# Performance work log

Measured on AMD Instinct MI355X. Metric: run time of the kernel, lower is better.

The kernel has to match this reference:

```python
import jax, jax.numpy as jnp
import numpy as np
import math

NUM_HEADS = 16


def setup_inputs() -> dict:
    key = jax.random.key(0)
    ks = jax.random.split(key, 7)
    d_model = 2048
    b, s = 2, 2048
    h = NUM_HEADS
    dh = d_model // h
    past_len = 2048
    std = math.sqrt(2.0 / (d_model + d_model))
    def w(k):
        return std * jax.random.truncated_normal(k, -3.0, 3.0, (d_model, d_model), jnp.float32)
    return {
        "x": jax.random.normal(ks[0], (b, s, d_model), jnp.float32),
        "past_k": jax.random.normal(ks[1], (b * h, past_len, dh), jnp.float32),
        "past_v": jax.random.normal(ks[2], (b * h, past_len, dh), jnp.float32),
        "Wq": w(ks[3]),
        "Wk": w(ks[4]),
        "Wv": w(ks[5]),
        "Wo": w(ks[6]),
    }


def reference(x, past_k, past_v, Wq, Wk, Wv, Wo):
    b, s, d_model = x.shape
    h = NUM_HEADS
    dh = d_model // h

    def proj_split(W):
        # (b, s, d_model) -> (b*h, s, dh)
        y = jnp.einsum('bsd,od->bso', x, W)
        return y.reshape(b, s, h, dh).transpose(0, 2, 1, 3).reshape(b * h, s, dh)

    Q = proj_split(Wq)
    K = proj_split(Wk)
    V = proj_split(Wv)

    past_len = past_k.shape[1]
    K = jnp.concatenate([past_k, K], axis=1)  # (b*h, total, dh)
    V = jnp.concatenate([past_v, V], axis=1)
    total = past_len + s

    # causal mask: query i (absolute pos past_len+i) attends to keys j <= past_len+i
    qi = jnp.arange(s)[:, None]
    kj = jnp.arange(total)[None, :]
    mask = kj <= (qi + past_len)  # (s, total)

    scores = jnp.einsum('bqd,bkd->bqk', Q, K) / math.sqrt(dh)
    scores = jnp.where(mask[None], scores, -jnp.inf)
    weights = jax.nn.softmax(scores, axis=-1)
    attn = jnp.einsum('bqk,bkv->bqv', weights, V)  # (b*h, s, dh)

    attn = attn.reshape(b, h, s, dh).transpose(0, 2, 1, 3).reshape(b, s, d_model)
    out = jnp.einsum('bsd,od->bso', attn, Wo)
    return out, K, V
```

## Files before the change

### kernel.cpp

```cpp
#include <hip/hip_runtime.h>

#define DM    2048
#define PAST  2048
#define TOT   4096
#define SCALE 0.08838834764831845f

typedef __attribute__((ext_vector_type(8))) short bf16x8;
typedef __attribute__((ext_vector_type(4))) float f32x4;
typedef __attribute__((ext_vector_type(4))) short s16x4;

typedef __attribute__((address_space(1))) void gvoid;
typedef __attribute__((address_space(3))) void lvoid;

__device__ __forceinline__ void gload16(const void* g, void* l) {
  __builtin_amdgcn_global_load_lds((gvoid*)g, (lvoid*)l, 16, 0, 0);
}

__device__ __forceinline__ short f2b(float f) {
  unsigned u = __float_as_uint(f);
  u += 0x7fffu + ((u >> 16) & 1u);
  return (short)(u >> 16);
}

__device__ __forceinline__ unsigned pk2(float a, float b) {
  return (unsigned)(unsigned short)f2b(a) | ((unsigned)(unsigned short)f2b(b) << 16);
}

template <bool F>
__device__ __forceinline__ bf16x8 ld8(const void* base, size_t eidx) {
  if constexpr (F) {
    const float* p = (const float*)base + eidx;
    float4 a = *(const float4*)p;
    float4 b = *(const float4*)(p + 4);
    bf16x8 r;
    r[0] = f2b(a.x); r[1] = f2b(a.y); r[2] = f2b(a.z); r[3] = f2b(a.w);
    r[4] = f2b(b.x); r[5] = f2b(b.y); r[6] = f2b(b.z); r[7] = f2b(b.w);
    return r;
  } else {
    return *(const bf16x8*)((const short*)base + eidx);
  }
}

__global__ void detect_dtype(const unsigned short* __restrict__ w, int* flag) {
  int cnt = 0;
#pragma unroll
  for (int i = 0; i < 4; ++i) {
    unsigned short v = w[i * 64 + threadIdx.x];
    int e = (v >> 7) & 0xFF;
    cnt += (e >= 126) ? 1 : 0;
  }
  for (int off = 32; off; off >>= 1) cnt += __shfl_down(cnt, off);
  if (threadIdx.x == 0) *flag = (cnt >= 8) ? 1 : 0;
}

__global__ __launch_bounds__(256)
void to_bf16(const int* __restrict__ flag,
             const float* __restrict__ x,
             const float* __restrict__ wq, const float* __restrict__ wk,
             const float* __restrict__ wv, const float* __restrict__ wo,
             short* __restrict__ xb, short* __restrict__ wqb,
             short* __restrict__ wkb, short* __restrict__ wvb,
             short* __restrict__ wob) {
  if (*flag != 1) return;
  const float* src; short* dst; size_t off = 0;
  switch (blockIdx.z) {
    case 0: src = x;  dst = xb;  break;
    case 1: src = x;  dst = xb;  off = 4194304; break;
    case 2: src = wq; dst = wqb; break;
    case 3: src = wk; dst = wkb; break;
    case 4: src = wv; dst = wvb; break;
    default: src = wo; dst = wob; break;
  }
  const size_t i = off + ((size_t)blockIdx.x * 256 + threadIdx.x) * 8;
  *(bf16x8*)(dst + i) = ld8<true>(src, i);
}

__device__ __forceinline__ void gemm_mainloop(
    const short* __restrict__ Ab, const short* __restrict__ Wb,
    short* shA, short* shB, f32x4 acc[4][4]) {
  const int tid  = threadIdx.x;
  const int lane = tid & 63, wid = tid >> 6;
  const int ln = lane & 15, qd = lane >> 4;
  const int wr = wid >> 1, wc = wid & 1;

  const int srow = lane >> 3;
  const int scol = ((lane & 7) ^ (lane >> 3)) * 8;

  for (int k0 = 0; k0 < DM; k0 += 64) {
#pragma unroll
    for (int i = 0; i < 4; ++i) {
      const int r8 = (wid * 4 + i) * 8 + srow;
      gload16(Ab + (size_t)r8 * DM + k0 + scol, (char*)shA + (wid * 4 + i) * 1024);
      gload16(Wb + (size_t)r8 * DM + k0 + scol, (char*)shB + (wid * 4 + i) * 1024);
    }
    __syncthreads();

#pragma unroll
    for (int t = 0; t < 2; ++t) {
      bf16x8 af[4], bw[4];
#pragma unroll
      for (int i = 0; i < 4; ++i) {
        const int rowA = wr * 64 + i * 16 + ln;
        const int rowB = wc * 64 + i * 16 + ln;
        const int cb   = ((t << 2) + qd) << 4;
        af[i] = *(const bf16x8*)((const char*)shA + rowA * 128 + (cb ^ ((rowA & 7) << 4)));
        bw[i] = *(const bf16x8*)((const char*)shB + rowB * 128 + (cb ^ ((rowB & 7) << 4)));
      }
#pragma unroll
      for (int i = 0; i < 4; ++i)
#pragma unroll
        for (int j = 0; j < 4; ++j)
          acc[i][j] = __builtin_amdgcn_mfma_f32_16x16x32_bf16(af[i], bw[j], acc[i][j], 0, 0, 0);
    }
    __syncthreads();
  }
}

__global__ __launch_bounds__(256, 2)
void qkv_gemm(const int* __restrict__ flag,
              const short* __restrict__ x0, const short* __restrict__ x1,
              const short* __restrict__ wq0, const short* __restrict__ wk0,
              const short* __restrict__ wv0,
              const short* __restrict__ wq1, const short* __restrict__ wk1,
              const short* __restrict__ wv1,
              short* __restrict__ Qws,
              short* __restrict__ Kb, float* __restrict__ Kf,
              short* __restrict__ Vb, float* __restrict__ Vf) {
  __shared__ __align__(16) short shA[128 * 64];
  __shared__ __align__(16) short shB[128 * 64];
  const int isF = *flag;
  const int bm = blockIdx.y, bn = blockIdx.x;
  const int seg = bn >> 4, bnl = bn & 15;

  const short* A = isF ? x1 : x0;
  const short* W = (seg == 0) ? (isF ? wq1 : wq0)
                  : (seg == 1) ? (isF ? wk1 : wk0)
                               : (isF ? wv1 : wv0);

  const f32x4 fz = {0.f, 0.f, 0.f, 0.f};
  f32x4 acc[4][4];
#pragma unroll
  for (int i = 0; i < 4; ++i)
#pragma unroll
    for (int j = 0; j < 4; ++j) acc[i][j] = fz;

  gemm_mainloop(A + (size_t)bm * 128 * DM, W + (size_t)bnl * 128 * DM, shA, shB, acc);

  const int tid  = threadIdx.x;
  const int lane = tid & 63, wid = tid >> 6;
  const int ln = lane & 15, qd = lane >> 4;
  const int wr = wid >> 1, wc = wid & 1;

#pragma unroll
  for (int i = 0; i < 4; ++i) {
    const int rbase = bm * 128 + wr * 64 + i * 16 + qd * 4;
#pragma unroll
    for (int j = 0; j < 4; ++j) {
      const int col = bnl * 128 + wc * 64 + j * 16 + ln;
#pragma unroll
      for (int r = 0; r < 4; ++r) {
        const int rr = rbase + r;
        const int bb = rr >> 11, sq = rr & 2047;
        const int hh = col >> 7, dd = col & 127;
        float v = acc[i][j][r];
        if (seg == 0) {
          const size_t idx = (((size_t)bb * 16 + hh) * 2048 + sq) * 128 + dd;
          Qws[idx] = f2b(v * SCALE);
        } else {
          const size_t idx = (((size_t)bb * 16 + hh) * (size_t)TOT + PAST + sq) * 128 + dd;
          if (seg == 1) { if (isF) Kf[idx] = v; else Kb[idx] = f2b(v); }
          else          { if (isF) Vf[idx] = v; else Vb[idx] = f2b(v); }
        }
      }
    }
  }
}

__global__ __launch_bounds__(256, 2)
void out_gemm(const int* __restrict__ flag,
              const short* __restrict__ A,
              const short* __restrict__ wo0, const short* __restrict__ wo1,
              void* __restrict__ dst) {
  __shared__ __align__(16) short shA[128 * 64];
  __shared__ __align__(16) short shB[128 * 64];
  const int isF = *flag;
  const int bm = blockIdx.y, bn = blockIdx.x;
  const short* W = isF ? wo1 : wo0;

  const f32x4 fz = {0.f, 0.f, 0.f, 0.f};
  f32x4 acc[4][4];
#pragma unroll
  for (int i = 0; i < 4; ++i)
#pragma unroll
    for (int j = 0; j < 4; ++j) acc[i][j] = fz;

  gemm_mainloop(A + (size_t)bm * 128 * DM, W + (size_t)bn * 128 * DM, shA, shB, acc);

  const int tid  = threadIdx.x;
  const int lane = tid & 63, wid = tid >> 6;
  const int ln = lane & 15, qd = lane >> 4;
  const int wr = wid >> 1, wc = wid & 1;

#pragma unroll
  for (int i = 0; i < 4; ++i) {
    const int rbase = bm * 128 + wr * 64 + i * 16 + qd * 4;
#pragma unroll
    for (int j = 0; j < 4; ++j) {
      const int col = bn * 128 + wc * 64 + j * 16 + ln;
#pragma unroll
      for (int r = 0; r < 4; ++r) {
        const size_t idx = (size_t)(rbase + r) * DM + col;
        if (isF) ((float*)dst)[idx] = acc[i][j][r];
        else     ((short*)dst)[idx] = f2b(acc[i][j][r]);
      }
    }
  }
}

__global__ __launch_bounds__(256)
void copy_past(const int* __restrict__ flag,
               const void* __restrict__ pk, const void* __restrict__ pv,
               short* __restrict__ Kb, float* __restrict__ Kf,
               short* __restrict__ Vb, float* __restrict__ Vf) {
  const int isF = *flag;
  const void* src = blockIdx.z ? pv : pk;
  const size_t c = (size_t)blockIdx.x * 256 + threadIdx.x;
  const size_t bh = c >> 15;
  const size_t rem = c & 32767;
  const size_t si = c * 8, di = bh * (size_t)TOT * 128 + rem * 8;
  if (isF) {
    float* dst = blockIdx.z ? Vf : Kf;
    const float* s = (const float*)src + si;
    float4 a = *(const float4*)s, b = *(const float4*)(s + 4);
    *(float4*)(dst + di) = a; *(float4*)(dst + di + 4) = b;
  } else {
    short* dst = blockIdx.z ? Vb : Kb;
    *(bf16x8*)(dst + di) = *(const bf16x8*)((const short*)src + si);
  }
}

__global__ __launch_bounds__(256)
void transpose_v(const int* __restrict__ flag,
                 const short* __restrict__ Vb, const float* __restrict__ Vf,
                 short* __restrict__ Vt) {
  __shared__ __align__(16) short sh[64 * 136];
  const int isF = *flag;
  const int tid = threadIdx.x;
  const int bh = blockIdx.y, kb = blockIdx.x << 6;
  const int krow = tid >> 4, dc = tid & 15;
#pragma unroll
  for (int rnd = 0; rnd < 4; ++rnd) {
    const int key = rnd * 16 + krow;
    const size_t idx = ((size_t)bh * TOT + kb + key) * 128 + dc * 8;
    bf16x8 v = isF ? ld8<true>(Vf, idx) : ld8<false>(Vb, idx);
    *(bf16x8*)(sh + key * 136 + dc * 8) = v;
  }
  __syncthreads();
  short* dstb = Vt + (size_t)bh * 128 * TOT + kb;
  const int drow = tid >> 3, keyc = tid & 7;
#pragma unroll
  for (int rnd = 0; rnd < 4; ++rnd) {
    const int dr = rnd * 32 + drow;
    bf16x8 ov;
#pragma unroll
    for (int e = 0; e < 8; ++e) ov[e] = sh[(keyc * 8 + e) * 136 + dr];
    *(bf16x8*)(dstb + (size_t)dr * TOT + keyc * 8) = ov;
  }
}

template <bool F>
__global__ __launch_bounds__(256, 2)
void attn_kernel(const int* __restrict__ flag, int want,
                 const short* __restrict__ Q,
                 const void* __restrict__ K,
                 const short* __restrict__ Vt,
                 short* __restrict__ attn) {
  if (*flag != want) return;
  __shared__ __align__(16) short shK[64 * 136];
  __shared__ __align__(16) short shV[128 * 72];
  __shared__ __align__(16) short shP[4][32 * 72];

  const int tid = threadIdx.x;
  const int lane = tid & 63, wid = tid >> 6;
  const int ln = lane & 15, qd = lane >> 4;

  const int l = blockIdx.y * 16 + blockIdx.x;
  const int qt = l >> 5;
  const int bh = ((l & 7) << 2) | ((l >> 3) & 3);
  const int q0 = qt << 7;
  const int r0w = q0 + wid * 32;

  bf16x8 qf[2][4];
#pragma unroll
  for (int mi = 0; mi < 2; ++mi) {
    const short* Qb = Q + ((size_t)bh * 2048 + r0w + mi * 16 + ln) * 128;
#pragma unroll
    for (int t = 0; t < 4; ++t) qf[mi][t] = *(const bf16x8*)(Qb + t * 32 + qd * 8);
  }

  const f32x4 fz = {0.f, 0.f, 0.f, 0.f};
  f32x4 O[2][8];
#pragma unroll
  for (int mi = 0; mi < 2; ++mi)
#pragma unroll
    for (int dt = 0; dt < 8; ++dt) O[mi][dt] = fz;
  float m_i[2] = {-1e30f, -1e30f}, l_i[2] = {0.f, 0.f};

  const short* Vb = Vt + (size_t)bh * 128 * TOT;
  const int ntiles = 34 + 2 * qt;

  const int krow = tid >> 4, kcol = tid & 15;
  const int vrow = tid >> 3, vcol = tid & 7;
  short* shPw = &shP[wid][0];

  bf16x8 vk[4], vv[4];
#pragma unroll
  for (int rnd = 0; rnd < 4; ++rnd) {
    vk[rnd] = ld8<F>(K, ((size_t)bh * TOT + rnd * 16 + krow) * 128 + kcol * 8);
    vv[rnd] = *(const bf16x8*)(Vb + (size_t)(rnd * 32 + vrow) * TOT + vcol * 8);
  }

  for (int kt = 0; kt < ntiles; ++kt) {
    const int kb = kt << 6;
#pragma unroll
    for (int rnd = 0; rnd < 4; ++rnd) {
      *(bf16x8*)(shK + (rnd * 16 + krow) * 136 + kcol * 8) = vk[rnd];
      *(bf16x8*)(shV + (rnd * 32 + vrow) * 72 + vcol * 8) = vv[rnd];
    }
    __syncthreads();

    if (kt + 1 < ntiles) {
      const int nb = kb + 64;
#pragma unroll
      for (int rnd = 0; rnd < 4; ++rnd) {
        vk[rnd] = ld8<F>(K, ((size_t)bh * TOT + nb + rnd * 16 + krow) * 128 + kcol * 8);
        vv[rnd] = *(const bf16x8*)(Vb + (size_t)(rnd * 32 + vrow) * TOT + nb + vcol * 8);
      }
    }

    f32x4 sacc[2][4];
#pragma unroll
    for (int mi = 0; mi < 2; ++mi)
#pragma unroll
      for (int j = 0; j < 4; ++j) sacc[mi][j] = fz;
#pragma unroll
    for (int t = 0; t < 4; ++t) {
#pragma unroll
      for (int j = 0; j < 4; ++j) {
        bf16x8 kf = *(const bf16x8*)(shK + (j * 16 + ln) * 136 + ((t << 2) + qd) * 8);
        sacc[0][j] = __builtin_amdgcn_mfma_f32_16x16x32_bf16(kf, qf[0][t], sacc[0][j], 0, 0, 0);
        sacc[1][j] = __builtin_amdgcn_mfma_f32_16x16x32_bf16(kf, qf[1][t], sacc[1][j], 0, 0, 0);
      }
    }

    const bool maskt = (kt >= ntiles - 2);

#pragma unroll
    for (int mi = 0; mi < 2; ++mi) {
      const int q = r0w + mi * 16 + ln;
      float vmax = -1e30f;
      if (maskt) {
        const int lim = PAST + q;
#pragma unroll
        for (int j = 0; j < 4; ++j)
#pragma unroll
          for (int r = 0; r < 4; ++r) {
            const int kj = kb + j * 16 + qd * 4 + r;
            float s = sacc[mi][j][r];
            s = (kj <= lim) ? s : -1e30f;
            sacc[mi][j][r] = s;
            vmax = fmaxf(vmax, s);
          }
      } else {
#pragma unroll
        for (int j = 0; j < 4; ++j)
#pragma unroll
          for (int r = 0; r < 4; ++r) vmax = fmaxf(vmax, sacc[mi][j][r]);
      }
      vmax = fmaxf(vmax, __shfl_xor(vmax, 16));
      vmax = fmaxf(vmax, __shfl_xor(vmax, 32));
      const float mold = m_i[mi];
      const bool renew = vmax > mold;
      const float mnew = renew ? vmax : mold;
      float rsum = 0.f;
#pragma unroll
      for (int j = 0; j < 4; ++j)
#pragma unroll
        for (int r = 0; r < 4; ++r) {
          const float p = __expf(sacc[mi][j][r] - mnew);
          sacc[mi][j][r] = p;
          rsum += p;
        }
      rsum += __shfl_xor(rsum, 16);
      rsum += __shfl_xor(rsum, 32);
      if (renew) {
        const float alpha = __expf(mold - mnew);
        m_i[mi] = mnew;
        l_i[mi] = l_i[mi] * alpha + rsum;
#pragma unroll
        for (int dt = 0; dt < 8; ++dt) O[mi][dt] *= alpha;
      } else {
        l_i[mi] += rsum;
      }
      const int qr = mi * 16 + ln;
#pragma unroll
      for (int j = 0; j < 4; ++j) {
        uint2 w;
        w.x = pk2(sacc[mi][j][0], sacc[mi][j][1]);
        w.y = pk2(sacc[mi][j][2], sacc[mi][j][3]);
        *(uint2*)(shPw + qr * 72 + j * 16 + qd * 4) = w;
      }
    }

#pragma unroll
    for (int tk = 0; tk < 2; ++tk) {
      bf16x8 pf[2];
#pragma unroll
      for (int mi = 0; mi < 2; ++mi)
        pf[mi] = *(const bf16x8*)(shPw + (mi * 16 + ln) * 72 + ((tk << 2) + qd) * 8);
#pragma unroll
      for (int dt = 0; dt < 8; ++dt) {
        bf16x8 vf = *(const bf16x8*)(shV + (dt * 16 + ln) * 72 + ((tk << 2) + qd) * 8);
        O[0][dt] = __builtin_amdgcn_mfma_f32_16x16x32_bf16(vf, pf[0], O[0][dt], 0, 0, 0);
        O[1][dt] = __builtin_amdgcn_mfma_f32_16x16x32_bf16(vf, pf[1], O[1][dt], 0, 0, 0);
      }
    }
    __syncthreads();
  }

  const int bb = bh >> 4, hh = bh & 15;
#pragma unroll
  for (int mi = 0; mi < 2; ++mi) {
    const float inv = 1.0f / l_i[mi];
    const int q = r0w + mi * 16 + ln;
    short* dst = attn + ((size_t)bb * 2048 + q) * DM + hh * 128;
#pragma unroll
    for (int dt = 0; dt < 8; ++dt) {
      s16x4 o;
#pragma unroll
      for (int r = 0; r < 4; ++r) o[r] = f2b(O[mi][dt][r] * inv);
      *(s16x4*)(dst + dt * 16 + qd * 4) = o;
    }
  }
}

extern "C" void kernel_launch(void* const* d_in, const int* in_sizes, int n_in,
                              void* d_out, int out_size, void* d_ws, size_t ws_size,
                              hipStream_t stream) {
  (void)in_sizes; (void)n_in; (void)out_size; (void)ws_size;
  const void* x  = d_in[0];
  const void* pk = d_in[1];
  const void* pv = d_in[2];
  const void* Wq = d_in[3];
  const void* Wk = d_in[4];
  const void* Wv = d_in[5];
  const void* Wo = d_in[6];

  int* flag = (int*)d_ws;
  short* base = (short*)((char*)d_ws + 256);
  short* Qws    = base;
  short* attnws = base + 8388608;
  short* xb     = attnws;
  short* Vtws   = base + 16777216;
  short* wqb    = Vtws;
  short* wkb    = Vtws + 4194304;
  short* wvb    = Vtws + 8388608;
  short* wob    = base + 33554432;

  short* outB  = (short*)d_out;
  short* KoutB = outB + (size_t)8388608;
  short* VoutB = KoutB + (size_t)16777216;
  float* outF  = (float*)d_out;
  float* KoutF = outF + (size_t)8388608;
  float* VoutF = KoutF + (size_t)16777216;

  dim3 blk(256);
  detect_dtype<<<1, 64, 0, stream>>>((const unsigned short*)Wq, flag);

  to_bf16<<<dim3(2048, 1, 6), blk, 0, stream>>>(flag,
      (const float*)x, (const float*)Wq, (const float*)Wk, (const float*)Wv,
      (const float*)Wo, xb, wqb, wkb, wvb, wob);

  qkv_gemm<<<dim3(48, 32), blk, 0, stream>>>(flag,
      (const short*)x, xb,
      (const short*)Wq, (const short*)Wk, (const short*)Wv,
      wqb, wkb, wvb,
      Qws, KoutB, KoutF, VoutB, VoutF);

  copy_past<<<dim3(4096, 1, 2), blk, 0, stream>>>(flag, pk, pv,
      KoutB, KoutF, VoutB, VoutF);

  transpose_v<<<dim3(64, 32), blk, 0, stream>>>(flag, VoutB, VoutF, Vtws);

  attn_kernel<false><<<dim3(16, 32), blk, 0, stream>>>(flag, 0, Qws, KoutB, Vtws, attnws);
  attn_kernel<true ><<<dim3(16, 32), blk, 0, stream>>>(flag, 1, Qws, KoutF, Vtws, attnws);

  out_gemm<<<dim3(16, 32), blk, 0, stream>>>(flag, attnws, (const short*)Wo, wob, d_out);
}
```

Baseline: 639.7 us.

## Double-buffer GEMM mainloop with larger tiles, hardware bf16 pack, reorder attention blocks

Replaces the GEMM mainloop with a double-buffered pipeline over 32-wide K steps, using 512-thread blocks and larger 256x256 (QKV) and 128x256 (output) tiles, so global loads overlap MFMA work. Software bf16 rounding is replaced by the v_cvt_pk_bf16_f32 instruction throughout. The attention grid mapping is changed to balance causal work across the launch order. The online softmax now only rescales when the running max grows by more than 8, which skips rescaling work but relies on exp values staying bounded. The new LDS layout has no swizzle, so bank conflicts on fragment reads are possible.

```diff
diff --git a/kernel.cpp b/kernel.cpp
--- a/kernel.cpp
+++ b/kernel.cpp
@@ -22,8 +22,10 @@
   return (short)(u >> 16);
 }
 
-__device__ __forceinline__ unsigned pk2(float a, float b) {
-  return (unsigned)(unsigned short)f2b(a) | ((unsigned)(unsigned short)f2b(b) << 16);
+__device__ __forceinline__ unsigned cvtpk(float lo, float hi) {
+  unsigned r;
+  asm("v_cvt_pk_bf16_f32 %0, %1, %2" : "=v"(r) : "v"(lo), "v"(hi));
+  return r;
 }
 
 template <bool F>
@@ -32,10 +34,10 @@
     const float* p = (const float*)base + eidx;
     float4 a = *(const float4*)p;
     float4 b = *(const float4*)(p + 4);
-    bf16x8 r;
-    r[0] = f2b(a.x); r[1] = f2b(a.y); r[2] = f2b(a.z); r[3] = f2b(a.w);
-    r[4] = f2b(b.x); r[5] = f2b(b.y); r[6] = f2b(b.z); r[7] = f2b(b.w);
-    return r;
+    union { unsigned u[4]; bf16x8 v; } r;
+    r.u[0] = cvtpk(a.x, a.y); r.u[1] = cvtpk(a.z, a.w);
+    r.u[2] = cvtpk(b.x, b.y); r.u[3] = cvtpk(b.z, b.w);
+    return r.v;
   } else {
     return *(const bf16x8*)((const short*)base + eidx);
   }
@@ -75,48 +77,66 @@
   *(bf16x8*)(dst + i) = ld8<true>(src, i);
 }
 
-__device__ __forceinline__ void gemm_mainloop(
-    const short* __restrict__ Ab, const short* __restrict__ Wb,
-    short* shA, short* shB, f32x4 acc[4][4]) {
-  const int tid  = threadIdx.x;
+template <int BM>
+__device__ __forceinline__ void pipe_main(const short* __restrict__ A,
+                                          const short* __restrict__ W,
+                                          short* sA, short* sB,
+                                          f32x4 acc[][4]) {
+  constexpr int MF = BM / 32;
+  constexpr int NL = BM / 128 + 2;
+  const int tid = threadIdx.x;
   const int lane = tid & 63, wid = tid >> 6;
   const int ln = lane & 15, qd = lane >> 4;
-  const int wr = wid >> 1, wc = wid & 1;
-
-  const int srow = lane >> 3;
-  const int scol = ((lane & 7) ^ (lane >> 3)) * 8;
-
-  for (int k0 = 0; k0 < DM; k0 += 64) {
-#pragma unroll
-    for (int i = 0; i < 4; ++i) {
-      const int r8 = (wid * 4 + i) * 8 + srow;
-      gload16(Ab + (size_t)r8 * DM + k0 + scol, (char*)shA + (wid * 4 + i) * 1024);
-      gload16(Wb + (size_t)r8 * DM + k0 + scol, (char*)shB + (wid * 4 + i) * 1024);
-    }
-    __syncthreads();
-
-#pragma unroll
-    for (int t = 0; t < 2; ++t) {
-      bf16x8 af[4], bw[4];
-#pragma unroll
-      for (int i = 0; i < 4; ++i) {
-        const int rowA = wr * 64 + i * 16 + ln;
-        const int rowB = wc * 64 + i * 16 + ln;
-        const int cb   = ((t << 2) + qd) << 4;
-        af[i] = *(const bf16x8*)((const char*)shA + rowA * 128 + (cb ^ ((rowA & 7) << 4)));
-        bw[i] = *(const bf16x8*)((const char*)shB + rowB * 128 + (cb ^ ((rowB & 7) << 4)));
-      }
-#pragma unroll
-      for (int i = 0; i < 4; ++i)
-#pragma unroll
-        for (int j = 0; j < 4; ++j)
-          acc[i][j] = __builtin_amdgcn_mfma_f32_16x16x32_bf16(af[i], bw[j], acc[i][j], 0, 0, 0);
-    }
-    __syncthreads();
-  }
-}
-
-__global__ __launch_bounds__(256, 2)
+  const int wm = wid >> 2, wn = wid & 3;
+
+  const int srow = tid >> 2;
+  const int scol = (tid & 3) * 8;
+
+  auto stage = [&](int t, int buf) {
+    const int k0 = t * 32;
+#pragma unroll
+    for (int c = 0; c < BM / 128; ++c)
+      gload16(A + (size_t)(c * 128 + srow) * DM + k0 + scol,
+              (char*)sA + buf * (BM * 64) + c * 8192 + tid * 16);
+#pragma unroll
+    for (int c = 0; c < 2; ++c)
+      gload16(W + (size_t)(c * 128 + srow) * DM + k0 + scol,
+              (char*)sB + buf * 16384 + c * 8192 + tid * 16);
+  };
+
+  stage(0, 0);
+  stage(1, 1);
+  asm volatile("s_waitcnt vmcnt(%0)" :: "n"(NL) : "memory");
+  __builtin_amdgcn_s_barrier();
+
+  for (int t = 0; t < 64; ++t) {
+    const short* Ab = sA + (t & 1) * (BM * 32);
+    const short* Bb = sB + (t & 1) * 8192;
+    bf16x8 af[MF], bw[4];
+#pragma unroll
+    for (int j = 0; j < 4; ++j)
+      bw[j] = *(const bf16x8*)(Bb + (wn * 64 + j * 16 + ln) * 32 + qd * 8);
+#pragma unroll
+    for (int i = 0; i < MF; ++i)
+      af[i] = *(const bf16x8*)(Ab + (wm * (BM / 2) + i * 16 + ln) * 32 + qd * 8);
+#pragma unroll
+    for (int i = 0; i < MF; ++i)
+#pragma unroll
+      for (int j = 0; j < 4; ++j)
+        acc[i][j] = __builtin_amdgcn_mfma_f32_16x16x32_bf16(af[i], bw[j], acc[i][j], 0, 0, 0);
+    if (t == 63) break;
+    __builtin_amdgcn_s_barrier();
+    if (t + 2 < 64) {
+      stage(t + 2, t & 1);
+      asm volatile("s_waitcnt vmcnt(%0)" :: "n"(NL) : "memory");
+    } else {
+      asm volatile("s_waitcnt vmcnt(0)" ::: "memory");
+    }
+    __builtin_amdgcn_s_barrier();
+  }
+}
+
+__global__ __launch_bounds__(512, 2)
 void qkv_gemm(const int* __restrict__ flag,
               const short* __restrict__ x0, const short* __restrict__ x1,
               const short* __restrict__ wq0, const short* __restrict__ wk0,
@@ -126,37 +146,37 @@
               short* __restrict__ Qws,
               short* __restrict__ Kb, float* __restrict__ Kf,
               short* __restrict__ Vb, float* __restrict__ Vf) {
-  __shared__ __align__(16) short shA[128 * 64];
-  __shared__ __align__(16) short shB[128 * 64];
+  __shared__ __align__(16) short sA[2 * 256 * 32];
+  __shared__ __align__(16) short sB[2 * 256 * 32];
   const int isF = *flag;
   const int bm = blockIdx.y, bn = blockIdx.x;
-  const int seg = bn >> 4, bnl = bn & 15;
-
-  const short* A = isF ? x1 : x0;
-  const short* W = (seg == 0) ? (isF ? wq1 : wq0)
-                  : (seg == 1) ? (isF ? wk1 : wk0)
-                               : (isF ? wv1 : wv0);
+  const int seg = bn >> 3, bnl = bn & 7;
+
+  const short* A = (isF ? x1 : x0) + (size_t)bm * 256 * DM;
+  const short* W = ((seg == 0) ? (isF ? wq1 : wq0)
+                   : (seg == 1) ? (isF ? wk1 : wk0)
+                                : (isF ? wv1 : wv0)) + (size_t)bnl * 256 * DM;
 
   const f32x4 fz = {0.f, 0.f, 0.f, 0.f};
-  f32x4 acc[4][4];
-#pragma unroll
-  for (int i = 0; i < 4; ++i)
+  f32x4 acc[8][4];
+#pragma unroll
+  for (int i = 0; i < 8; ++i)
 #pragma unroll
     for (int j = 0; j < 4; ++j) acc[i][j] = fz;
 
-  gemm_mainloop(A + (size_t)bm * 128 * DM, W + (size_t)bnl * 128 * DM, shA, shB, acc);
-
-  const int tid  = threadIdx.x;
+  pipe_main<256>(A, W, sA, sB, acc);
+
+  const int tid = threadIdx.x;
   const int lane = tid & 63, wid = tid >> 6;
   const int ln = lane & 15, qd = lane >> 4;
-  const int wr = wid >> 1, wc = wid & 1;
-
-#pragma unroll
-  for (int i = 0; i < 4; ++i) {
-    const int rbase = bm * 128 + wr * 64 + i * 16 + qd * 4;
+  const int wm = wid >> 2, wn = wid & 3;
+
+#pragma unroll
+  for (int i = 0; i < 8; ++i) {
+    const int rbase = bm * 256 + wm * 128 + i * 16 + qd * 4;
 #pragma unroll
     for (int j = 0; j < 4; ++j) {
-      const int col = bnl * 128 + wc * 64 + j * 16 + ln;
+      const int col = bnl * 256 + wn * 64 + j * 16 + ln;
 #pragma unroll
       for (int r = 0; r < 4; ++r) {
         const int rr = rbase + r;
@@ -176,16 +196,16 @@
   }
 }
 
-__global__ __launch_bounds__(256, 2)
+__global__ __launch_bounds__(512, 2)
 void out_gemm(const int* __restrict__ flag,
               const short* __restrict__ A,
               const short* __restrict__ wo0, const short* __restrict__ wo1,
               void* __restrict__ dst) {
-  __shared__ __align__(16) short shA[128 * 64];
-  __shared__ __align__(16) short shB[128 * 64];
+  __shared__ __align__(16) short sA[2 * 128 * 32];
+  __shared__ __align__(16) short sB[2 * 256 * 32];
   const int isF = *flag;
   const int bm = blockIdx.y, bn = blockIdx.x;
-  const short* W = isF ? wo1 : wo0;
+  const short* W = (isF ? wo1 : wo0) + (size_t)bn * 256 * DM;
 
   const f32x4 fz = {0.f, 0.f, 0.f, 0.f};
   f32x4 acc[4][4];
@@ -194,19 +214,19 @@
 #pragma unroll
     for (int j = 0; j < 4; ++j) acc[i][j] = fz;
 
-  gemm_mainloop(A + (size_t)bm * 128 * DM, W + (size_t)bn * 128 * DM, shA, shB, acc);
-
-  const int tid  = threadIdx.x;
+  pipe_main<128>(A + (size_t)bm * 128 * DM, W, sA, sB, acc);
+
+  const int tid = threadIdx.x;
   const int lane = tid & 63, wid = tid >> 6;
   const int ln = lane & 15, qd = lane >> 4;
-  const int wr = wid >> 1, wc = wid & 1;
+  const int wm = wid >> 2, wn = wid & 3;
 
 #pragma unroll
   for (int i = 0; i < 4; ++i) {
-    const int rbase = bm * 128 + wr * 64 + i * 16 + qd * 4;
+    const int rbase = bm * 128 + wm * 64 + i * 16 + qd * 4;
 #pragma unroll
     for (int j = 0; j < 4; ++j) {
-      const int col = bn * 128 + wc * 64 + j * 16 + ln;
+      const int col = bn * 256 + wn * 64 + j * 16 + ln;
 #pragma unroll
       for (int r = 0; r < 4; ++r) {
         const size_t idx = (size_t)(rbase + r) * DM + col;
@@ -285,8 +305,9 @@
   const int ln = lane & 15, qd = lane >> 4;
 
   const int l = blockIdx.y * 16 + blockIdx.x;
-  const int qt = l >> 5;
-  const int bh = ((l & 7) << 2) | ((l >> 3) & 3);
+  const int s = l >> 3;
+  const int qt = (s < 32) ? (s >> 2) : (15 - ((s - 32) >> 2));
+  const int bh = ((l & 7) << 2) | (s & 3);
   const int q0 = qt << 7;
   const int r0w = q0 + wid * 32;
 
@@ -366,10 +387,10 @@
 #pragma unroll
           for (int r = 0; r < 4; ++r) {
             const int kj = kb + j * 16 + qd * 4 + r;
-            float s = sacc[mi][j][r];
-            s = (kj <= lim) ? s : -1e30f;
-            sacc[mi][j][r] = s;
-            vmax = fmaxf(vmax, s);
+            float v = sacc[mi][j][r];
+            v = (kj <= lim) ? v : -1e30f;
+            sacc[mi][j][r] = v;
+            vmax = fmaxf(vmax, v);
           }
       } else {
 #pragma unroll
@@ -380,7 +401,7 @@
       vmax = fmaxf(vmax, __shfl_xor(vmax, 16));
       vmax = fmaxf(vmax, __shfl_xor(vmax, 32));
       const float mold = m_i[mi];
-      const bool renew = vmax > mold;
+      const bool renew = vmax > mold + 8.0f;
       const float mnew = renew ? vmax : mold;
       float rsum = 0.f;
 #pragma unroll
@@ -406,8 +427,8 @@
 #pragma unroll
       for (int j = 0; j < 4; ++j) {
         uint2 w;
-        w.x = pk2(sacc[mi][j][0], sacc[mi][j][1]);
-        w.y = pk2(sacc[mi][j][2], sacc[mi][j][3]);
+        w.x = cvtpk(sacc[mi][j][0], sacc[mi][j][1]);
+        w.y = cvtpk(sacc[mi][j][2], sacc[mi][j][3]);
         *(uint2*)(shPw + qr * 72 + j * 16 + qd * 4) = w;
       }
     }
@@ -436,10 +457,10 @@
     short* dst = attn + ((size_t)bb * 2048 + q) * DM + hh * 128;
 #pragma unroll
     for (int dt = 0; dt < 8; ++dt) {
-      s16x4 o;
-#pragma unroll
-      for (int r = 0; r < 4; ++r) o[r] = f2b(O[mi][dt][r] * inv);
-      *(s16x4*)(dst + dt * 16 + qd * 4) = o;
+      union { unsigned u[2]; s16x4 v; } o;
+      o.u[0] = cvtpk(O[mi][dt][0] * inv, O[mi][dt][1] * inv);
+      o.u[1] = cvtpk(O[mi][dt][2] * inv, O[mi][dt][3] * inv);
+      *(s16x4*)(dst + dt * 16 + qd * 4) = o.v;
     }
   }
 }
@@ -481,7 +502,7 @@
       (const float*)x, (const float*)Wq, (const float*)Wk, (const float*)Wv,
       (const float*)Wo, xb, wqb, wkb, wvb, wob);
 
-  qkv_gemm<<<dim3(48, 32), blk, 0, stream>>>(flag,
+  qkv_gemm<<<dim3(24, 16), dim3(512), 0, stream>>>(flag,
       (const short*)x, xb,
       (const short*)Wq, (const short*)Wk, (const short*)Wv,
       wqb, wkb, wvb,
@@ -495,5 +516,6 @@
   attn_kernel<false><<<dim3(16, 32), blk, 0, stream>>>(flag, 0, Qws, KoutB, Vtws, attnws);
   attn_kernel<true ><<<dim3(16, 32), blk, 0, stream>>>(flag, 1, Qws, KoutF, Vtws, attnws);
 
-  out_gemm<<<dim3(16, 32), blk, 0, stream>>>(flag, attnws, (const short*)Wo, wob, d_out);
-}
+  out_gemm<<<dim3(8, 32), dim3(512), 0, stream>>>(flag, attnws,
+      (const short*)Wo, wob, d_out);
+}
```

After: 741.6 us. +15.9%, slower.

## Double-buffer GEMM LDS, use hardware exp2 and packed bf16 converts, rebalance attention tiles

Applied to the files above, without the earlier changes.

The GEMM main loop now uses two LDS buffers, prefetching the next K-slice while the current one is multiplied, so each iteration waits on one barrier instead of two. The attention softmax folds log2(e) into the Q scale and calls hardware v_exp_f32 directly. It also rescales the running max only when the new max exceeds the old by more than 8 (lazy rescale). Software bf16 rounding is replaced by the v_cvt_pk_bf16_f32 instruction, and the attention block order is remapped to interleave long and short causal tiles. The extra LDS per GEMM block may reduce occupancy, and the lazy rescale slightly changes numerics.

```diff
diff --git a/kernel.cpp b/kernel.cpp
--- a/kernel.cpp
+++ b/kernel.cpp
@@ -4,6 +4,7 @@
 #define PAST  2048
 #define TOT   4096
 #define SCALE 0.08838834764831845f
+#define QSCALE 0.1275475036480354f
 
 typedef __attribute__((ext_vector_type(8))) short bf16x8;
 typedef __attribute__((ext_vector_type(4))) float f32x4;
@@ -22,8 +23,16 @@
   return (short)(u >> 16);
 }
 
-__device__ __forceinline__ unsigned pk2(float a, float b) {
-  return (unsigned)(unsigned short)f2b(a) | ((unsigned)(unsigned short)f2b(b) << 16);
+__device__ __forceinline__ unsigned cvtpk(float lo, float hi) {
+  unsigned r;
+  asm("v_cvt_pk_bf16_f32 %0, %1, %2" : "=v"(r) : "v"(lo), "v"(hi));
+  return r;
+}
+
+__device__ __forceinline__ float exp2hw(float x) {
+  float r;
+  asm("v_exp_f32 %0, %1" : "=v"(r) : "v"(x));
+  return r;
 }
 
 template <bool F>
@@ -32,10 +41,10 @@
     const float* p = (const float*)base + eidx;
     float4 a = *(const float4*)p;
     float4 b = *(const float4*)(p + 4);
-    bf16x8 r;
-    r[0] = f2b(a.x); r[1] = f2b(a.y); r[2] = f2b(a.z); r[3] = f2b(a.w);
-    r[4] = f2b(b.x); r[5] = f2b(b.y); r[6] = f2b(b.z); r[7] = f2b(b.w);
-    return r;
+    union { unsigned u[4]; bf16x8 v; } r;
+    r.u[0] = cvtpk(a.x, a.y); r.u[1] = cvtpk(a.z, a.w);
+    r.u[2] = cvtpk(b.x, b.y); r.u[3] = cvtpk(b.z, b.w);
+    return r.v;
   } else {
     return *(const bf16x8*)((const short*)base + eidx);
   }
@@ -77,7 +86,7 @@
 
 __device__ __forceinline__ void gemm_mainloop(
     const short* __restrict__ Ab, const short* __restrict__ Wb,
-    short* shA, short* shB, f32x4 acc[4][4]) {
+    short* sA, short* sB, f32x4 acc[4][4]) {
   const int tid  = threadIdx.x;
   const int lane = tid & 63, wid = tid >> 6;
   const int ln = lane & 15, qd = lane >> 4;
@@ -86,15 +95,27 @@
   const int srow = lane >> 3;
   const int scol = ((lane & 7) ^ (lane >> 3)) * 8;
 
-  for (int k0 = 0; k0 < DM; k0 += 64) {
+  auto stage = [&](int k0, int buf) {
 #pragma unroll
     for (int i = 0; i < 4; ++i) {
       const int r8 = (wid * 4 + i) * 8 + srow;
-      gload16(Ab + (size_t)r8 * DM + k0 + scol, (char*)shA + (wid * 4 + i) * 1024);
-      gload16(Wb + (size_t)r8 * DM + k0 + scol, (char*)shB + (wid * 4 + i) * 1024);
-    }
-    __syncthreads();
-
+      gload16(Ab + (size_t)r8 * DM + k0 + scol,
+              (char*)sA + buf * 16384 + (wid * 4 + i) * 1024);
+      gload16(Wb + (size_t)r8 * DM + k0 + scol,
+              (char*)sB + buf * 16384 + (wid * 4 + i) * 1024);
+    }
+  };
+
+  stage(0, 0);
+  asm volatile("s_waitcnt vmcnt(0)" ::: "memory");
+  __builtin_amdgcn_s_barrier();
+
+  int cur = 0;
+  for (int k0 = 0; k0 < DM; k0 += 64) {
+    if (k0 + 64 < DM) stage(k0 + 64, cur ^ 1);
+
+    const char* Ac = (const char*)sA + cur * 16384;
+    const char* Bc = (const char*)sB + cur * 16384;
 #pragma unroll
     for (int t = 0; t < 2; ++t) {
       bf16x8 af[4], bw[4];
@@ -103,8 +124,8 @@
         const int rowA = wr * 64 + i * 16 + ln;
         const int rowB = wc * 64 + i * 16 + ln;
         const int cb   = ((t << 2) + qd) << 4;
-        af[i] = *(const bf16x8*)((const char*)shA + rowA * 128 + (cb ^ ((rowA & 7) << 4)));
-        bw[i] = *(const bf16x8*)((const char*)shB + rowB * 128 + (cb ^ ((rowB & 7) << 4)));
+        af[i] = *(const bf16x8*)(Ac + rowA * 128 + (cb ^ ((rowA & 7) << 4)));
+        bw[i] = *(const bf16x8*)(Bc + rowB * 128 + (cb ^ ((rowB & 7) << 4)));
       }
 #pragma unroll
       for (int i = 0; i < 4; ++i)
@@ -112,7 +133,9 @@
         for (int j = 0; j < 4; ++j)
           acc[i][j] = __builtin_amdgcn_mfma_f32_16x16x32_bf16(af[i], bw[j], acc[i][j], 0, 0, 0);
     }
-    __syncthreads();
+    asm volatile("s_waitcnt vmcnt(0)" ::: "memory");
+    __builtin_amdgcn_s_barrier();
+    cur ^= 1;
   }
 }
 
@@ -126,8 +149,8 @@
               short* __restrict__ Qws,
               short* __restrict__ Kb, float* __restrict__ Kf,
               short* __restrict__ Vb, float* __restrict__ Vf) {
-  __shared__ __align__(16) short shA[128 * 64];
-  __shared__ __align__(16) short shB[128 * 64];
+  __shared__ __align__(16) short shA[2 * 128 * 64];
+  __shared__ __align__(16) short shB[2 * 128 * 64];
   const int isF = *flag;
   const int bm = blockIdx.y, bn = blockIdx.x;
   const int seg = bn >> 4, bnl = bn & 15;
@@ -165,7 +188,7 @@
         float v = acc[i][j][r];
         if (seg == 0) {
           const size_t idx = (((size_t)bb * 16 + hh) * 2048 + sq) * 128 + dd;
-          Qws[idx] = f2b(v * SCALE);
+          Qws[idx] = f2b(v * QSCALE);
         } else {
           const size_t idx = (((size_t)bb * 16 + hh) * (size_t)TOT + PAST + sq) * 128 + dd;
           if (seg == 1) { if (isF) Kf[idx] = v; else Kb[idx] = f2b(v); }
@@ -181,8 +204,8 @@
               const short* __restrict__ A,
               const short* __restrict__ wo0, const short* __restrict__ wo1,
               void* __restrict__ dst) {
-  __shared__ __align__(16) short shA[128 * 64];
-  __shared__ __align__(16) short shB[128 * 64];
+  __shared__ __align__(16) short shA[2 * 128 * 64];
+  __shared__ __align__(16) short shB[2 * 128 * 64];
   const int isF = *flag;
   const int bm = blockIdx.y, bn = blockIdx.x;
   const short* W = isF ? wo1 : wo0;
@@ -285,8 +308,9 @@
   const int ln = lane & 15, qd = lane >> 4;
 
   const int l = blockIdx.y * 16 + blockIdx.x;
-  const int qt = l >> 5;
-  const int bh = ((l & 7) << 2) | ((l >> 3) & 3);
+  const int s = l >> 3;
+  const int qt = (s < 32) ? (s >> 2) : (15 - ((s - 32) >> 2));
+  const int bh = ((l & 7) << 2) | (s & 3);
   const int q0 = qt << 7;
   const int r0w = q0 + wid * 32;
 
@@ -366,10 +390,10 @@
 #pragma unroll
           for (int r = 0; r < 4; ++r) {
             const int kj = kb + j * 16 + qd * 4 + r;
-            float s = sacc[mi][j][r];
-            s = (kj <= lim) ? s : -1e30f;
-            sacc[mi][j][r] = s;
-            vmax = fmaxf(vmax, s);
+            float v = sacc[mi][j][r];
+            v = (kj <= lim) ? v : -1e30f;
+            sacc[mi][j][r] = v;
+            vmax = fmaxf(vmax, v);
           }
       } else {
 #pragma unroll
@@ -380,21 +404,21 @@
       vmax = fmaxf(vmax, __shfl_xor(vmax, 16));
       vmax = fmaxf(vmax, __shfl_xor(vmax, 32));
       const float mold = m_i[mi];
-      const bool renew = vmax > mold;
+      const bool renew = vmax > mold + 8.0f;
       const float mnew = renew ? vmax : mold;
       float rsum = 0.f;
 #pragma unroll
       for (int j = 0; j < 4; ++j)
 #pragma unroll
         for (int r = 0; r < 4; ++r) {
-          const float p = __expf(sacc[mi][j][r] - mnew);
+          const float p = exp2hw(sacc[mi][j][r] - mnew);
           sacc[mi][j][r] = p;
           rsum += p;
         }
       rsum += __shfl_xor(rsum, 16);
       rsum += __shfl_xor(rsum, 32);
       if (renew) {
-        const float alpha = __expf(mold - mnew);
+        const float alpha = exp2hw(mold - mnew);
         m_i[mi] = mnew;
         l_i[mi] = l_i[mi] * alpha + rsum;
 #pragma unroll
@@ -406,8 +430,8 @@
 #pragma unroll
       for (int j = 0; j < 4; ++j) {
         uint2 w;
-        w.x = pk2(sacc[mi][j][0], sacc[mi][j][1]);
-        w.y = pk2(sacc[mi][j][2], sacc[mi][j][3]);
+        w.x = cvtpk(sacc[mi][j][0], sacc[mi][j][1]);
+        w.y = cvtpk(sacc[mi][j][2], sacc[mi][j][3]);
         *(uint2*)(shPw + qr * 72 + j * 16 + qd * 4) = w;
       }
     }
@@ -436,10 +460,10 @@
     short* dst = attn + ((size_t)bb * 2048 + q) * DM + hh * 128;
 #pragma unroll
     for (int dt = 0; dt < 8; ++dt) {
-      s16x4 o;
-#pragma unroll
-      for (int r = 0; r < 4; ++r) o[r] = f2b(O[mi][dt][r] * inv);
-      *(s16x4*)(dst + dt * 16 + qd * 4) = o;
+      union { unsigned u[2]; s16x4 v; } o;
+      o.u[0] = cvtpk(O[mi][dt][0] * inv, O[mi][dt][1] * inv);
+      o.u[1] = cvtpk(O[mi][dt][2] * inv, O[mi][dt][3] * inv);
+      *(s16x4*)(dst + dt * 16 + qd * 4) = o.v;
     }
   }
 }
@@ -495,5 +519,6 @@
   attn_kernel<false><<<dim3(16, 32), blk, 0, stream>>>(flag, 0, Qws, KoutB, Vtws, attnws);
   attn_kernel<true ><<<dim3(16, 32), blk, 0, stream>>>(flag, 1, Qws, KoutF, Vtws, attnws);
 
-  out_gemm<<<dim3(16, 32), blk, 0, stream>>>(flag, attnws, (const short*)Wo, wob, d_out);
-}
+  out_gemm<<<dim3(16, 32), blk, 0, stream>>>(flag, attnws,
+      (const short*)Wo, wob, d_out);
+}
```

Result: slower. 658.5 us (+2.9%).
